# Kernel optimization log

Measured on AMD Instinct MI355X. Metric: run time of the kernel, lower is better.

Reference implementation:

```python
import jax, jax.numpy as jnp
import numpy as np

D_MODEL = 1024
TDS = 64
B, S = 8, 2048
DIN = D_MODEL + TDS   # 1088
DH = D_MODEL // 2     # 512


def setup_inputs() -> dict:
    key = jax.random.key(0)
    ks = jax.random.split(key, 6)
    sc = 1.0 / np.sqrt(DIN)
    return {
        "time_features": jax.random.normal(ks[0], (B, S, D_MODEL), jnp.float32),
        "env_info": jax.random.normal(ks[1], (B, TDS), jnp.float32),
        "Wq": jax.random.normal(ks[2], (DIN, DH), jnp.float32) * sc,
        "bq": jnp.zeros((DH,), jnp.float32),
        "Wk": jax.random.normal(ks[3], (DIN, DH), jnp.float32) * sc,
        "bk": jnp.zeros((DH,), jnp.float32),
        "Wv": jax.random.normal(ks[4], (DIN, DH), jnp.float32) * sc,
        "bv": jnp.zeros((DH,), jnp.float32),
        "Wg": jax.random.normal(ks[5], (DIN, 1), jnp.float32) * sc,
        "bg": jnp.zeros((1,), jnp.float32),
    }


def reference(time_features, env_info, Wq, bq, Wk, bk, Wv, bv, Wg, bg):
    b, s, _ = time_features.shape
    env = jnp.broadcast_to(env_info[:, None, :], (b, s, env_info.shape[-1]))
    x = jnp.concatenate([time_features, env], axis=2)  # [B,S,DIN]
    q = x @ Wq + bq                                    # [B,S,DH]
    k = x @ Wk + bk
    v = x @ Wv + bv
    gate = jax.nn.sigmoid(x @ Wg + bg)                 # [B,S,1]
    scores = jnp.einsum('bqd,bkd->bqk', q, k) / jnp.sqrt(jnp.float32(D_MODEL))
    gated = scores * gate                              # gate broadcasts over key dim
    attn = jax.nn.softmax(gated, axis=-1)
    return jnp.einsum('bqk,bkd->bqd', attn, v)         # [B,S,DH]
```

## Files before the change

kernel.cpp:

```cpp
#include <hip/hip_runtime.h>
#include <stdint.h>

typedef __attribute__((ext_vector_type(8))) __bf16 bf16x8;
typedef __attribute__((ext_vector_type(4))) __bf16 bf16x4;
typedef __attribute__((ext_vector_type(4))) float  f32x4;

#define DEV __device__ __forceinline__

DEV void gload16(const void* g, void* l) {
  __builtin_amdgcn_global_load_lds((const __attribute__((address_space(1))) uint32_t*)g,
                                   (__attribute__((address_space(3))) uint32_t*)l,
                                   16, 0, 0);
}

DEV f32x4 mfma16(bf16x8 a, bf16x8 b, f32x4 c) {
  return __builtin_amdgcn_mfma_f32_16x16x32_bf16(a, b, c, 0, 0, 0);
}

#define XB_OFF   0UL
#define S_OFF    0UL
#define Q_OFF    33554432UL
#define K_OFF    50331648UL
#define VT_OFF   67108864UL
#define WT_OFF   83886080UL
#define ENVQ_OFF 87031808UL
#define GATE_OFF 87080960UL
#define S8_OFF   87146496UL

__global__ __launch_bounds__(256) void k_xbgate(
    const float* __restrict__ tf, const float* __restrict__ env,
    const float* __restrict__ Wg, const float* __restrict__ bg,
    __bf16* __restrict__ xbb, float* __restrict__ gate) {
  const int row = blockIdx.x;
  const int t   = threadIdx.x;
  const int b   = row >> 11;
  const float4 v  = ((const float4*)(tf + (size_t)row * 1024))[t];
  const float4 wv = ((const float4*)Wg)[t];
  float dot = v.x * wv.x + v.y * wv.y + v.z * wv.z + v.w * wv.w;
  bf16x4 o; o.x = (__bf16)v.x; o.y = (__bf16)v.y; o.z = (__bf16)v.z; o.w = (__bf16)v.w;
  *(bf16x4*)(xbb + (size_t)row * 1024 + t * 4) = o;
  if (t < 16) {
    const float4 e  = ((const float4*)(env + b * 64))[t];
    const float4 we = ((const float4*)Wg)[256 + t];
    dot += e.x * we.x + e.y * we.y + e.z * we.z + e.w * we.w;
  }
  #pragma unroll
  for (int m = 1; m < 64; m <<= 1) dot += __shfl_xor(dot, m, 64);
  __shared__ float red[4];
  if ((t & 63) == 0) red[t >> 6] = dot;
  __syncthreads();
  if (t == 0) {
    const float d = red[0] + red[1] + red[2] + red[3] + bg[0];
    gate[row] = 0.03125f / (1.0f + __expf(-d));
  }
}

__global__ __launch_bounds__(256) void k_wt(
    const float* __restrict__ Wq, const float* __restrict__ Wk, const float* __restrict__ Wv,
    __bf16* __restrict__ Wt) {
  __shared__ float tile[64][65];
  const int kt = blockIdx.x;
  const int ct = blockIdx.y;
  const int which = blockIdx.z;
  const float* W = (which == 0) ? Wq : (which == 1) ? Wk : Wv;
  const int t = threadIdx.x;
  const int k0 = kt * 64, c0 = ct * 64;
  #pragma unroll
  for (int j = 0; j < 4; ++j) {
    const int rr = (t >> 4) + j * 16;
    const float4 v4 = *(const float4*)(W + (size_t)(k0 + rr) * 512 + c0 + (t & 15) * 4);
    tile[rr][(t & 15) * 4 + 0] = v4.x;
    tile[rr][(t & 15) * 4 + 1] = v4.y;
    tile[rr][(t & 15) * 4 + 2] = v4.z;
    tile[rr][(t & 15) * 4 + 3] = v4.w;
  }
  __syncthreads();
  #pragma unroll
  for (int j = 0; j < 4; ++j) {
    const int nl = (t >> 4) + j * 16;
    const int kl = (t & 15) * 4;
    bf16x4 o;
    o.x = (__bf16)tile[kl + 0][nl];
    o.y = (__bf16)tile[kl + 1][nl];
    o.z = (__bf16)tile[kl + 2][nl];
    o.w = (__bf16)tile[kl + 3][nl];
    *(bf16x4*)(Wt + (size_t)(which * 512 + c0 + nl) * 1024 + k0 + kl) = o;
  }
}

__global__ __launch_bounds__(256) void k_envq(
    const float* __restrict__ env,
    const float* __restrict__ Wq, const float* __restrict__ Wk, const float* __restrict__ Wv,
    const float* __restrict__ bq, const float* __restrict__ bk, const float* __restrict__ bv,
    float* __restrict__ envq) {
  const int n = blockIdx.x * 256 + threadIdx.x;
  const int b = blockIdx.y;
  const int which = n >> 9, col = n & 511;
  const float* W    = (which == 0) ? Wq : (which == 1) ? Wk : Wv;
  const float* bias = (which == 0) ? bq : (which == 1) ? bk : bv;
  float s = bias[col];
  #pragma unroll 8
  for (int kk = 0; kk < 64; ++kk)
    s += env[b * 64 + kk] * W[(size_t)(1024 + kk) * 512 + col];
  envq[b * 1536 + n] = s;
}

__global__ __launch_bounds__(256, 3) void k_gemm(
    const __bf16* __restrict__ xbb, const __bf16* __restrict__ Wt,
    const float* __restrict__ envq, const float* __restrict__ gate,
    __bf16* __restrict__ q, __bf16* __restrict__ k, __bf16* __restrict__ vT) {
  __shared__ alignas(16) __bf16 SM[16384];
  __bf16* As = SM;
  __bf16* Bs = SM + 8192;
  const int id = blockIdx.x;
  const int xcd = id & 7, local = id >> 3;
  const int bm = xcd * 16 + (local & 15);
  const int bn = local >> 4;
  const int tid = threadIdx.x, w = tid >> 6, lane = tid & 63;
  const int g = lane >> 4, l15 = lane & 15;
  const int wm = w >> 1, wn = w & 1;
  f32x4 acc[4][4] = {};
  const char* Ab = (const char*)(xbb + (size_t)bm * 128 * 1024);
  const char* Bb = (const char*)(Wt + (size_t)bn * 128 * 1024);

  for (int kt = 0; kt < 16; ++kt) {
    const int k0b = kt * 128;
    #pragma unroll
    for (int i = 0; i < 4; ++i) {
      const int L = i * 4096 + w * 1024 + lane * 16;
      const int row = L >> 7;
      const int ch = (L >> 4) & 7;
      const int sch = ch ^ (row & 7);
      gload16(Ab + (size_t)row * 2048 + k0b + sch * 16, (char*)As + L);
      gload16(Bb + (size_t)row * 2048 + k0b + sch * 16, (char*)Bs + L);
    }
    __syncthreads();
    #pragma unroll
    for (int kk = 0; kk < 2; ++kk) {
      bf16x8 aF[4], bF[4];
      #pragma unroll
      for (int i = 0; i < 4; ++i) {
        const int rowa = wm * 64 + i * 16 + l15;
        const int cha = (kk * 4 + g) ^ (rowa & 7);
        aF[i] = *(const bf16x8*)((const char*)As + rowa * 128 + cha * 16);
        const int rowb = wn * 64 + i * 16 + l15;
        const int chb = (kk * 4 + g) ^ (rowb & 7);
        bF[i] = *(const bf16x8*)((const char*)Bs + rowb * 128 + chb * 16);
      }
      #pragma unroll
      for (int i = 0; i < 4; ++i)
        #pragma unroll
        for (int j = 0; j < 4; ++j)
          acc[i][j] = mfma16(aF[i], bF[j], acc[i][j]);
    }
    __syncthreads();
  }

  const int which = bn >> 2;
  const int batch = bm >> 4;
  if (which < 2) {
    __bf16* outp = (which == 0) ? q : k;
    const int ncolbase = bn * 128 + wn * 64 - which * 512;
    #pragma unroll
    for (int i = 0; i < 4; ++i) {
      #pragma unroll
      for (int r = 0; r < 4; ++r) {
        const int mrow = bm * 128 + wm * 64 + i * 16 + g * 4 + r;
        const float gt = (which == 0) ? gate[mrow] : 1.0f;
        #pragma unroll
        for (int j = 0; j < 4; ++j) {
          const int ncol = ncolbase + j * 16 + l15;
          float val = acc[i][j][r] + envq[batch * 1536 + bn * 128 + wn * 64 + j * 16 + l15];
          if (which == 0) val *= gt;
          outp[(size_t)mrow * 512 + ncol] = (__bf16)val;
        }
      }
    }
  } else {
    #pragma unroll
    for (int j = 0; j < 4; ++j) {
      const int ncol = wn * 64 + j * 16 + l15;
      const float bv = envq[batch * 1536 + bn * 128 + ncol];
      const int sw = (ncol & 7) << 3;
      #pragma unroll
      for (int i = 0; i < 4; ++i) {
        const int mbase = wm * 64 + i * 16 + g * 4;
        bf16x4 pk;
        pk.x = (__bf16)(acc[i][j][0] + bv);
        pk.y = (__bf16)(acc[i][j][1] + bv);
        pk.z = (__bf16)(acc[i][j][2] + bv);
        pk.w = (__bf16)(acc[i][j][3] + bv);
        *(bf16x4*)(SM + ncol * 128 + (mbase ^ sw)) = pk;
      }
    }
    __syncthreads();
    const int colL = tid & 127, h = tid >> 7;
    const __bf16* src = SM + colL * 128;
    const int sw = (colL & 7) << 3;
    __bf16* dst = vT + ((size_t)batch * 512 + (bn - 8) * 128 + colL) * 2048
                     + (bm & 15) * 128 + h * 64;
    #pragma unroll
    for (int c = 0; c < 8; ++c) {
      const int m0 = h * 64 + c * 8;
      *(bf16x8*)(dst + c * 8) = *(const bf16x8*)(src + (m0 ^ sw));
    }
  }
}

template<int NB>
__global__ __launch_bounds__(256, 3) void k_sexp(
    const __bf16* __restrict__ q, const __bf16* __restrict__ kg,
    __bf16* __restrict__ S) {
  __shared__ alignas(16) __bf16 As[8192];
  __shared__ alignas(16) __bf16 Bs[8192];
  const int id = blockIdx.x;
  int batch, t;
  if (NB == 8) { batch = id & 7;        t = id >> 3; }
  else         { batch = (id & 7) >> 1; t = ((id >> 3) << 1) | (id & 1); }
  const int mt = t & 15, nt = t >> 4;
  const int tid = threadIdx.x, w = tid >> 6, lane = tid & 63;
  const int g = lane >> 4, l15 = lane & 15;
  const int wm = w >> 1, wn = w & 1;
  f32x4 acc[4][4] = {};
  const char* Ab = (const char*)(q  + ((size_t)batch * 2048 + mt * 128) * 512);
  const char* Bb = (const char*)(kg + ((size_t)batch * 2048 + nt * 128) * 512);

  for (int kt = 0; kt < 8; ++kt) {
    const int k0b = kt * 128;
    #pragma unroll
    for (int i = 0; i < 4; ++i) {
      const int L = i * 4096 + w * 1024 + lane * 16;
      const int row = L >> 7;
      const int ch = (L >> 4) & 7;
      const int sch = ch ^ (row & 7);
      gload16(Ab + (size_t)row * 1024 + k0b + sch * 16, (char*)As + L);
      gload16(Bb + (size_t)row * 1024 + k0b + sch * 16, (char*)Bs + L);
    }
    __syncthreads();
    #pragma unroll
    for (int kk = 0; kk < 2; ++kk) {
      bf16x8 aF[4], bF[4];
      #pragma unroll
      for (int i = 0; i < 4; ++i) {
        const int rowa = wm * 64 + i * 16 + l15;
        const int cha = (kk * 4 + g) ^ (rowa & 7);
        aF[i] = *(const bf16x8*)((const char*)As + rowa * 128 + cha * 16);
        const int rowb = wn * 64 + i * 16 + l15;
        const int chb = (kk * 4 + g) ^ (rowb & 7);
        bF[i] = *(const bf16x8*)((const char*)Bs + rowb * 128 + chb * 16);
      }
      #pragma unroll
      for (int i = 0; i < 4; ++i)
        #pragma unroll
        for (int j = 0; j < 4; ++j)
          acc[i][j] = mfma16(aF[i], bF[j], acc[i][j]);
    }
    __syncthreads();
  }

  __bf16* Srow = S + (size_t)batch * 2048 * 2048;
  #pragma unroll
  for (int i = 0; i < 4; ++i) {
    #pragma unroll
    for (int r = 0; r < 4; ++r) {
      const int mrow = mt * 128 + wm * 64 + i * 16 + g * 4 + r;
      #pragma unroll
      for (int j = 0; j < 4; ++j) {
        const int ncol = nt * 128 + wn * 64 + j * 16 + l15;
        Srow[(size_t)mrow * 2048 + ncol] = (__bf16)__expf(acc[i][j][r]);
      }
    }
  }
}

template<int NB>
__global__ __launch_bounds__(256, 3) void k_pv(
    const __bf16* __restrict__ S, const __bf16* __restrict__ vT,
    float* __restrict__ out) {
  __shared__ alignas(16) __bf16 As[8192];
  __shared__ alignas(16) __bf16 Bs[8192];
  const int id = blockIdx.x;
  int batch, mt, nt;
  if (NB == 8) { batch = id & 7; const int h = id >> 3; mt = h & 15; nt = h >> 4; }
  else { batch = (id & 7) >> 1; const int h = ((id >> 3) << 1) | (id & 1); mt = h & 15; nt = h >> 4; }
  const int tid = threadIdx.x, w = tid >> 6, lane = tid & 63;
  const int g = lane >> 4, l15 = lane & 15;
  const int wm = w >> 1, wn = w & 1;
  f32x4 acc[4][4] = {};
  f32x4 l_acc[4] = {};
  bf16x8 ones;
  #pragma unroll
  for (int j = 0; j < 8; ++j) ones[j] = (__bf16)1.0f;

  const char* Ab = (const char*)(S  + ((size_t)batch * 2048 + mt * 128) * 2048);
  const char* Bb = (const char*)(vT + ((size_t)batch * 512 + nt * 128) * 2048);

  for (int kt = 0; kt < 32; ++kt) {
    const int k0b = kt * 128;
    #pragma unroll
    for (int i = 0; i < 4; ++i) {
      const int L = i * 4096 + w * 1024 + lane * 16;
      const int row = L >> 7, ch = (L >> 4) & 7, sch = ch ^ (row & 7);
      gload16(Ab + (size_t)row * 4096 + k0b + sch * 16, (char*)As + L);
      gload16(Bb + (size_t)row * 4096 + k0b + sch * 16, (char*)Bs + L);
    }
    __syncthreads();
    #pragma unroll
    for (int kk = 0; kk < 2; ++kk) {
      bf16x8 aF[4], bF[4];
      #pragma unroll
      for (int i = 0; i < 4; ++i) {
        const int rowa = wm * 64 + i * 16 + l15;
        const int cha = (kk * 4 + g) ^ (rowa & 7);
        aF[i] = *(const bf16x8*)((const char*)As + rowa * 128 + cha * 16);
        const int rowb = wn * 64 + i * 16 + l15;
        const int chb = (kk * 4 + g) ^ (rowb & 7);
        bF[i] = *(const bf16x8*)((const char*)Bs + rowb * 128 + chb * 16);
      }
      #pragma unroll
      for (int i = 0; i < 4; ++i) {
        #pragma unroll
        for (int j = 0; j < 4; ++j)
          acc[i][j] = mfma16(aF[i], bF[j], acc[i][j]);
        l_acc[i] = mfma16(aF[i], ones, l_acc[i]);
      }
    }
    __syncthreads();
  }

  #pragma unroll
  for (int i = 0; i < 4; ++i) {
    #pragma unroll
    for (int r = 0; r < 4; ++r) {
      const size_t mrow = (size_t)batch * 2048 + mt * 128 + wm * 64 + i * 16 + g * 4 + r;
      const float inv = 1.0f / l_acc[i][r];
      #pragma unroll
      for (int j = 0; j < 4; ++j) {
        const int ncol = nt * 128 + wn * 64 + j * 16 + l15;
        out[mrow * 512 + ncol] = acc[i][j][r] * inv;
      }
    }
  }
}

extern "C" void kernel_launch(void* const* d_in, const int* in_sizes, int n_in,
                              void* d_out, int out_size, void* d_ws, size_t ws_size,
                              hipStream_t stream) {
  const float* tf  = (const float*)d_in[0];
  const float* env = (const float*)d_in[1];
  const float* Wq  = (const float*)d_in[2];
  const float* bq  = (const float*)d_in[3];
  const float* Wk  = (const float*)d_in[4];
  const float* bk  = (const float*)d_in[5];
  const float* Wv  = (const float*)d_in[6];
  const float* bv  = (const float*)d_in[7];
  const float* Wg  = (const float*)d_in[8];
  const float* bg  = (const float*)d_in[9];
  float* out = (float*)d_out;
  char* ws = (char*)d_ws;

  __bf16* xbb  = (__bf16*)(ws + XB_OFF);
  __bf16* Sbuf = (__bf16*)(ws + S_OFF);
  __bf16* qb   = (__bf16*)(ws + Q_OFF);
  __bf16* kb   = (__bf16*)(ws + K_OFF);
  __bf16* vT   = (__bf16*)(ws + VT_OFF);
  __bf16* Wt   = (__bf16*)(ws + WT_OFF);
  float* envq  = (float*)(ws + ENVQ_OFF);
  float* gate  = (float*)(ws + GATE_OFF);

  k_xbgate<<<dim3(16384), dim3(256), 0, stream>>>(tf, env, Wg, bg, xbb, gate);
  k_wt<<<dim3(16, 8, 3), dim3(256), 0, stream>>>(Wq, Wk, Wv, Wt);
  k_envq<<<dim3(6, 8), dim3(256), 0, stream>>>(env, Wq, Wk, Wv, bq, bk, bv, envq);
  k_gemm<<<dim3(1536), dim3(256), 0, stream>>>(xbb, Wt, envq, gate, qb, kb, vT);

  if (ws_size >= S8_OFF + 67108864UL) {
    __bf16* S8 = (__bf16*)(ws + S8_OFF);
    k_sexp<8><<<dim3(2048), dim3(256), 0, stream>>>(qb, kb, S8);
    k_pv<8>  <<<dim3(512),  dim3(256), 0, stream>>>(S8, vT, out);
  } else {
    const size_t hb = 4UL * 2048 * 512;
    const size_t hv = 4UL * 512 * 2048;
    const size_t ho = 4UL * 2048 * 512;
    k_sexp<4><<<dim3(1024), dim3(256), 0, stream>>>(qb, kb, Sbuf);
    k_pv<4>  <<<dim3(256),  dim3(256), 0, stream>>>(Sbuf, vT, out);
    k_sexp<4><<<dim3(1024), dim3(256), 0, stream>>>(qb + hb, kb + hb, Sbuf);
    k_pv<4>  <<<dim3(256),  dim3(256), 0, stream>>>(Sbuf, vT + hv, out + ho);
  }
}
```

Before: 162.9 us.

## Compute softmax row sums in score kernel instead of extra MFMAs in PV

Row sums of exp(scores) are now accumulated in the score-exponent kernel's epilogue using shuffles and shared memory, then written as per-tile partials. A small reduction kernel turns them into inverse sums, which the PV kernel reads in place of its ones-vector MFMAs, removing about 20% of its matrix instructions. This adds a launch, partial-sum traffic, a barrier in the score epilogue, and sums taken in fp32 rather than from the bf16-rounded values. The GEMM kernel's launch bound also goes from 3 to 4 blocks per CU.

```diff
diff --git a/kernel.cpp b/kernel.cpp
--- a/kernel.cpp
+++ b/kernel.cpp
@@ -25,7 +25,9 @@
 #define WT_OFF   83886080UL
 #define ENVQ_OFF 87031808UL
 #define GATE_OFF 87080960UL
-#define S8_OFF   87146496UL
+#define LP_OFF   87146496UL
+#define INVL_OFF 89243648UL
+#define S8_OFF   89309184UL
 
 __global__ __launch_bounds__(256) void k_xbgate(
     const float* __restrict__ tf, const float* __restrict__ env,
@@ -105,7 +107,7 @@
   envq[b * 1536 + n] = s;
 }
 
-__global__ __launch_bounds__(256, 3) void k_gemm(
+__global__ __launch_bounds__(256, 4) void k_gemm(
     const __bf16* __restrict__ xbb, const __bf16* __restrict__ Wt,
     const float* __restrict__ envq, const float* __restrict__ gate,
     __bf16* __restrict__ q, __bf16* __restrict__ k, __bf16* __restrict__ vT) {
@@ -210,7 +212,7 @@
 template<int NB>
 __global__ __launch_bounds__(256, 3) void k_sexp(
     const __bf16* __restrict__ q, const __bf16* __restrict__ kg,
-    __bf16* __restrict__ S) {
+    __bf16* __restrict__ S, float* __restrict__ l_part) {
   __shared__ alignas(16) __bf16 As[8192];
   __shared__ alignas(16) __bf16 Bs[8192];
   const int id = blockIdx.x;
@@ -259,24 +261,57 @@
   }
 
   __bf16* Srow = S + (size_t)batch * 2048 * 2048;
+  float p[4][4];
   #pragma unroll
   for (int i = 0; i < 4; ++i) {
     #pragma unroll
     for (int r = 0; r < 4; ++r) {
       const int mrow = mt * 128 + wm * 64 + i * 16 + g * 4 + r;
+      float s0 = 0.f;
       #pragma unroll
       for (int j = 0; j < 4; ++j) {
+        const float e = __expf(acc[i][j][r]);
+        s0 += e;
         const int ncol = nt * 128 + wn * 64 + j * 16 + l15;
-        Srow[(size_t)mrow * 2048 + ncol] = (__bf16)__expf(acc[i][j][r]);
-      }
-    }
-  }
+        Srow[(size_t)mrow * 2048 + ncol] = (__bf16)e;
+      }
+      s0 += __shfl_xor(s0, 1, 64);
+      s0 += __shfl_xor(s0, 2, 64);
+      s0 += __shfl_xor(s0, 4, 64);
+      s0 += __shfl_xor(s0, 8, 64);
+      p[i][r] = s0;
+    }
+  }
+  float* lx = (float*)As;
+  if (l15 == 0) {
+    #pragma unroll
+    for (int i = 0; i < 4; ++i)
+      #pragma unroll
+      for (int r = 0; r < 4; ++r)
+        lx[(wm * 2 + wn) * 64 + i * 16 + g * 4 + r] = p[i][r];
+  }
+  __syncthreads();
+  if (wn == 0) {
+    const int row64 = lane;
+    const float v = lx[(wm * 2 + 0) * 64 + row64] + lx[(wm * 2 + 1) * 64 + row64];
+    l_part[((size_t)batch * 2048 + mt * 128 + wm * 64 + row64) * 16 + nt] = v;
+  }
+}
+
+__global__ __launch_bounds__(256) void k_lred(const float* __restrict__ l_part,
+                                              float* __restrict__ inv_l) {
+  const int row = blockIdx.x * 256 + threadIdx.x;
+  const float4* lp = (const float4*)(l_part + (size_t)row * 16);
+  const float4 a = lp[0], b = lp[1], c = lp[2], d = lp[3];
+  const float s = ((a.x + a.y) + (a.z + a.w)) + ((b.x + b.y) + (b.z + b.w))
+                + ((c.x + c.y) + (c.z + c.w)) + ((d.x + d.y) + (d.z + d.w));
+  inv_l[row] = 1.0f / s;
 }
 
 template<int NB>
 __global__ __launch_bounds__(256, 3) void k_pv(
     const __bf16* __restrict__ S, const __bf16* __restrict__ vT,
-    float* __restrict__ out) {
+    const float* __restrict__ inv_l, float* __restrict__ out) {
   __shared__ alignas(16) __bf16 As[8192];
   __shared__ alignas(16) __bf16 Bs[8192];
   const int id = blockIdx.x;
@@ -287,10 +322,6 @@
   const int g = lane >> 4, l15 = lane & 15;
   const int wm = w >> 1, wn = w & 1;
   f32x4 acc[4][4] = {};
-  f32x4 l_acc[4] = {};
-  bf16x8 ones;
-  #pragma unroll
-  for (int j = 0; j < 8; ++j) ones[j] = (__bf16)1.0f;
 
   const char* Ab = (const char*)(S  + ((size_t)batch * 2048 + mt * 128) * 2048);
   const char* Bb = (const char*)(vT + ((size_t)batch * 512 + nt * 128) * 2048);
@@ -318,12 +349,10 @@
         bF[i] = *(const bf16x8*)((const char*)Bs + rowb * 128 + chb * 16);
       }
       #pragma unroll
-      for (int i = 0; i < 4; ++i) {
+      for (int i = 0; i < 4; ++i)
         #pragma unroll
         for (int j = 0; j < 4; ++j)
           acc[i][j] = mfma16(aF[i], bF[j], acc[i][j]);
-        l_acc[i] = mfma16(aF[i], ones, l_acc[i]);
-      }
     }
     __syncthreads();
   }
@@ -333,7 +362,7 @@
     #pragma unroll
     for (int r = 0; r < 4; ++r) {
       const size_t mrow = (size_t)batch * 2048 + mt * 128 + wm * 64 + i * 16 + g * 4 + r;
-      const float inv = 1.0f / l_acc[i][r];
+      const float inv = inv_l[mrow];
       #pragma unroll
       for (int j = 0; j < 4; ++j) {
         const int ncol = nt * 128 + wn * 64 + j * 16 + l15;
@@ -367,6 +396,8 @@
   __bf16* Wt   = (__bf16*)(ws + WT_OFF);
   float* envq  = (float*)(ws + ENVQ_OFF);
   float* gate  = (float*)(ws + GATE_OFF);
+  float* lpart = (float*)(ws + LP_OFF);
+  float* invl  = (float*)(ws + INVL_OFF);
 
   k_xbgate<<<dim3(16384), dim3(256), 0, stream>>>(tf, env, Wg, bg, xbb, gate);
   k_wt<<<dim3(16, 8, 3), dim3(256), 0, stream>>>(Wq, Wk, Wv, Wt);
@@ -375,15 +406,18 @@
 
   if (ws_size >= S8_OFF + 67108864UL) {
     __bf16* S8 = (__bf16*)(ws + S8_OFF);
-    k_sexp<8><<<dim3(2048), dim3(256), 0, stream>>>(qb, kb, S8);
-    k_pv<8>  <<<dim3(512),  dim3(256), 0, stream>>>(S8, vT, out);
+    k_sexp<8><<<dim3(2048), dim3(256), 0, stream>>>(qb, kb, S8, lpart);
+    k_lred<<<dim3(64), dim3(256), 0, stream>>>(lpart, invl);
+    k_pv<8>  <<<dim3(512),  dim3(256), 0, stream>>>(S8, vT, invl, out);
   } else {
     const size_t hb = 4UL * 2048 * 512;
     const size_t hv = 4UL * 512 * 2048;
     const size_t ho = 4UL * 2048 * 512;
-    k_sexp<4><<<dim3(1024), dim3(256), 0, stream>>>(qb, kb, Sbuf);
-    k_pv<4>  <<<dim3(256),  dim3(256), 0, stream>>>(Sbuf, vT, out);
-    k_sexp<4><<<dim3(1024), dim3(256), 0, stream>>>(qb + hb, kb + hb, Sbuf);
-    k_pv<4>  <<<dim3(256),  dim3(256), 0, stream>>>(Sbuf, vT + hv, out + ho);
-  }
-}
+    k_sexp<4><<<dim3(1024), dim3(256), 0, stream>>>(qb, kb, Sbuf, lpart);
+    k_lred<<<dim3(32), dim3(256), 0, stream>>>(lpart, invl);
+    k_pv<4>  <<<dim3(256),  dim3(256), 0, stream>>>(Sbuf, vT, invl, out);
+    k_sexp<4><<<dim3(1024), dim3(256), 0, stream>>>(qb + hb, kb + hb, Sbuf, lpart);
+    k_lred<<<dim3(32), dim3(256), 0, stream>>>(lpart, invl);
+    k_pv<4>  <<<dim3(256),  dim3(256), 0, stream>>>(Sbuf, vT + hv, invl, out + ho);
+  }
+}
```

Result: slower. 166.7 us (+2.3%).
